# Performance work log

Hardware: AMD Instinct MI355X
Metric: run time of the kernel (lower is better)

The kernel has to match this reference:

```python
import jax, jax.numpy as jnp
import numpy as np

B, T, C = 8, 1024, 1024
H, HKV = 16, 4
HD = C // H            # 64
G = H // HKV           # 4 (GQA group size)
CAP = 50.0
THETA = 10000.0
EPS = 1e-6


def _rope_tables(t, d, theta):
    inv_freq = 1.0 / (theta ** (jnp.arange(0, d, 2, dtype=jnp.float32) / d))
    pos = jnp.arange(t, dtype=jnp.float32)
    freqs = jnp.outer(pos, inv_freq)            # [T, d/2]
    return jnp.cos(freqs), jnp.sin(freqs)


def _rmsnorm(x, w):
    var = jnp.mean(x * x, axis=-1, keepdims=True)
    return x * jax.lax.rsqrt(var + EPS) * w


def _apply_rope(x, cos, sin):
    # x: [B, T, h, HD]; cos/sin: [T, HD/2]
    d = x.shape[-1] // 2
    x1, x2 = x[..., :d], x[..., d:]
    c = cos[None, :, None, :]
    s = sin[None, :, None, :]
    return jnp.concatenate([x1 * c + x2 * s, -x1 * s + x2 * c], axis=-1)


def setup_inputs() -> dict:
    key = jax.random.key(0)
    ks = jax.random.split(key, 6)
    std = 0.02
    x = jax.random.normal(ks[0], (B, T, C), dtype=jnp.float32)
    w_q = jax.random.normal(ks[1], (C, C), dtype=jnp.float32) * std
    w_kv = jax.random.normal(ks[2], (2 * C // G, C), dtype=jnp.float32) * std  # [512, 1024]
    w_c = jax.random.normal(ks[3], (C, C), dtype=jnp.float32) * std
    q_norm_w = jnp.ones((HD,), dtype=jnp.float32)
    k_norm_w = jnp.ones((HD,), dtype=jnp.float32)
    return {"x": x, "w_q": w_q, "w_kv": w_kv, "w_c": w_c,
            "q_norm_w": q_norm_w, "k_norm_w": k_norm_w}


def reference(x, w_q, w_kv, w_c, q_norm_w, k_norm_w):
    # projections (no bias)
    q = (x @ w_q.T).reshape(B, T, H, HD)
    kv = (x @ w_kv.T).reshape(B, T, 2, HKV, HD)
    k, v = kv[:, :, 0], kv[:, :, 1]            # [B, T, HKV, HD]

    # RMSNorm on q/k heads
    q = _rmsnorm(q, q_norm_w)
    k = _rmsnorm(k, k_norm_w)

    # RoPE (half-split rotation, as in apply_rotary_emb)
    cos, sin = _rope_tables(T, HD, THETA)
    q = _apply_rope(q, cos, sin)
    k = _apply_rope(k, cos, sin)

    # GQA layout: heads grouped over kv heads (equiv to repeat_interleave)
    q = q.transpose(0, 2, 1, 3).reshape(B, HKV, G, T, HD)   # [B, nkv, G, T, HD]
    k = k.transpose(0, 2, 1, 3)                             # [B, nkv, T, HD]
    v = v.transpose(0, 2, 1, 3)

    scale = 1.0 / jnp.sqrt(jnp.float32(HD))
    att = jnp.einsum('bngqd,bnkd->bngqk', q, k) * scale     # [B, nkv, G, T, T]
    att = CAP * jnp.tanh(att / CAP)                          # soft logit cap

    causal = jnp.arange(T)[:, None] >= jnp.arange(T)[None, :]  # [T, T]
    att = jnp.where(causal[None, None, None], att, -jnp.inf)
    att = jax.nn.softmax(att, axis=-1)

    y = jnp.einsum('bngqk,bnkd->bngqd', att, v)             # [B, nkv, G, T, HD]
    y = y.reshape(B, H, T, HD).transpose(0, 2, 1, 3).reshape(B, T, C)
    return y @ w_c.T
```

## Files before the change

### kernel.cpp

```cpp
#include <hip/hip_runtime.h>
#include <math.h>

#define BB 8
#define TT 1024
#define CC 1024
#define HH 16
#define HKV 4
#define HD 64
#define MM (BB*TT)
#define LOG2E 1.4426950408889634f

typedef __attribute__((ext_vector_type(8))) short bf16x8;
typedef __attribute__((ext_vector_type(4))) float f32x4;

__device__ __forceinline__ float b2f(unsigned short x){
    union{unsigned int i; float f;} u; u.i = ((unsigned int)x)<<16; return u.f;
}
__device__ __forceinline__ unsigned short f2b(float f){
    union{float f; unsigned int i;} u; u.f = f;
    unsigned int r = u.i + 0x7fffu + ((u.i>>16)&1u);
    return (unsigned short)(r>>16);
}

#define GLD16(gp, lp) __builtin_amdgcn_global_load_lds( \
    (__attribute__((address_space(1))) void*)(gp), \
    (__attribute__((address_space(3))) void*)(lp), 16, 0, 0)

__global__ __launch_bounds__(256) void cvt_all(const float* __restrict__ x,
                                               const float* __restrict__ w_q,
                                               const float* __restrict__ w_kv,
                                               const float* __restrict__ w_c,
                                               unsigned short* __restrict__ xb,
                                               unsigned short* __restrict__ wqkvb,
                                               unsigned short* __restrict__ wcb){
    int i = blockIdx.x*256 + threadIdx.x;
    const float* src; unsigned short* dst; int off;
    if (i < 2097152)      { src = x;    dst = xb;              off = i; }
    else if (i < 2359296) { src = w_q;  dst = wqkvb;           off = i - 2097152; }
    else if (i < 2490368) { src = w_kv; dst = wqkvb + 1048576; off = i - 2359296; }
    else                  { src = w_c;  dst = wcb;             off = i - 2490368; }
    float4 f = ((const float4*)src)[off];
    ushort4 o;
    o.x = f2b(f.x); o.y = f2b(f.y); o.z = f2b(f.z); o.w = f2b(f.w);
    ((ushort4*)dst)[off] = o;
}

template<int BF16OUT>
__global__ __launch_bounds__(256, 4) void gemm_bt(const unsigned short* __restrict__ A,
                                                  const unsigned short* __restrict__ Bt,
                                                  void* __restrict__ Cc,
                                                  int M, int N, int K){
    __shared__ __align__(16) unsigned short As[128*64];
    __shared__ __align__(16) unsigned short Bs[128*64];
    const int tid  = threadIdx.x;
    const int wid  = tid >> 6;
    const int lane = tid & 63;
    const int wm   = wid >> 1;
    const int wn   = wid & 1;
    const int l16  = lane & 15;
    const int quad = lane >> 4;

    int bm, bn;
    {
        int gx = gridDim.x;
        int p  = blockIdx.y * gx + blockIdx.x;
        int nb = gx * gridDim.y;
        int l  = (p & 7) * (nb >> 3) + (p >> 3);
        bn = (l % gx) * 128;
        bm = (l / gx) * 128;
    }

    const unsigned short* ga[4]; const unsigned short* gb[4];
    char* la[4]; char* lb[4];
    {
        int rbase = tid >> 3, c_lds = tid & 7;
        #pragma unroll
        for (int it = 0; it < 4; ++it){
            int row = it*32 + rbase;
            int cg  = c_lds ^ (row & 7);
            ga[it] = A  + (size_t)(bm+row)*K + cg*8;
            gb[it] = Bt + (size_t)(bn+row)*K + cg*8;
            la[it] = (char*)As + (size_t)(it*256 + tid)*16;
            lb[it] = (char*)Bs + (size_t)(it*256 + tid)*16;
        }
    }

    f32x4 acc[4][4] = {};

    for (int k0 = 0; k0 < K; k0 += 64){
        __syncthreads();
        #pragma unroll
        for (int it = 0; it < 4; ++it){
            GLD16(ga[it] + k0, la[it]);
            GLD16(gb[it] + k0, lb[it]);
        }
        __syncthreads();

        #pragma unroll
        for (int kh = 0; kh < 2; ++kh){
            bf16x8 af[4], bfr[4];
            #pragma unroll
            for (int i = 0; i < 4; ++i){
                int row = wm*64 + i*16 + l16;
                int ch  = (kh*4 + quad) ^ (row & 7);
                af[i] = *(const bf16x8*)(As + row*64 + ch*8);
            }
            #pragma unroll
            for (int j = 0; j < 4; ++j){
                int row = wn*64 + j*16 + l16;
                int ch  = (kh*4 + quad) ^ (row & 7);
                bfr[j] = *(const bf16x8*)(Bs + row*64 + ch*8);
            }
            #pragma unroll
            for (int i = 0; i < 4; ++i)
                #pragma unroll
                for (int j = 0; j < 4; ++j)
                    acc[i][j] = __builtin_amdgcn_mfma_f32_16x16x32_bf16(af[i], bfr[j], acc[i][j], 0, 0, 0);
        }
    }

    #pragma unroll
    for (int i = 0; i < 4; ++i){
        int row0 = wm*64 + i*16 + quad*4;
        #pragma unroll
        for (int j = 0; j < 4; ++j){
            int col = bn + wn*64 + j*16 + l16;
            #pragma unroll
            for (int r = 0; r < 4; ++r){
                if (BF16OUT)
                    ((unsigned short*)Cc)[(size_t)(bm + row0 + r)*N + col] = f2b(acc[i][j][r]);
                else
                    ((float*)Cc)[(size_t)(bm + row0 + r)*N + col] = acc[i][j][r];
            }
        }
    }
}

__global__ __launch_bounds__(256) void prep_kv(const unsigned short* __restrict__ QKVb,
                                               const float* __restrict__ kw,
                                               unsigned short* __restrict__ ka,
                                               unsigned short* __restrict__ vat){
    __shared__ unsigned short tile[64][72];
    const int tid = threadIdx.x;
    const int tblk = blockIdx.x, n = blockIdx.y, b = blockIdx.z;

    #pragma unroll
    for (int it = 0; it < 2; ++it){
        int i = it*256 + tid;
        int r = i >> 3, c = i & 7;
        uint4 v = *(const uint4*)(QKVb + ((size_t)(b*TT + tblk*64 + r))*1536 + 1280 + n*64 + c*8);
        *(uint4*)(&tile[r][c*8]) = v;
    }

    {
        const int rr = tid >> 6, lane = tid & 63;
        const float kwl = kw[lane];
        const float invf = exp2f(-(float)(lane & 31) * (13.287712379549449f/32.0f));
        #pragma unroll 4
        for (int p = 0; p < 16; ++p){
            int t = tblk*64 + p*4 + rr;
            float val = b2f(QKVb[((size_t)(b*TT + t))*1536 + 1024 + n*64 + lane]);
            float ss = val*val;
            #pragma unroll
            for (int off = 32; off > 0; off >>= 1) ss += __shfl_xor(ss, off, 64);
            float normed = val * rsqrtf(ss*(1.0f/64.0f) + 1e-6f) * kwl;
            float s, c;
            sincosf((float)t * invf, &s, &c);
            float other = __shfl_xor(normed, 32, 64);
            float outv = (lane < 32) ? (normed*c + other*s) : (-other*s + normed*c);
            ka[(((size_t)(b*HKV + n))*TT + t)*HD + lane] = f2b(outv);
        }
    }

    __syncthreads();
    const int d = tid >> 2, tseg = tid & 3;
    unsigned short tmp[16];
    #pragma unroll
    for (int i = 0; i < 16; ++i) tmp[i] = tile[tseg*16 + i][d];
    size_t off = (((size_t)(b*HKV + n))*HD + d)*TT + tblk*64 + tseg*16;
    *(uint4*)(vat + off)     = *(const uint4*)tmp;
    *(uint4*)(vat + off + 8) = *(const uint4*)(tmp + 8);
}

__global__ __launch_bounds__(512, 4) void attn_mfma(const unsigned short* __restrict__ QKVb,
                                                    const unsigned short* __restrict__ ka,
                                                    const unsigned short* __restrict__ vat,
                                                    const float* __restrict__ qw,
                                                    unsigned short* __restrict__ ya){
    __shared__ __align__(16) unsigned short Ks[64*64];
    __shared__ __align__(16) unsigned short Vts[64*64];
    __shared__ __align__(16) unsigned short Ps[8][32*72];

    const int tid = threadIdx.x;
    const int wave = tid >> 6, lane = tid & 63;
    const int l16 = lane & 15, quad = lane >> 4;
    const int n = blockIdx.x, b = blockIdx.y, iz = blockIdx.z;
    const int ib = (iz < 8) ? iz : 23 - iz;
    const int head = wave & 3, sub = wave >> 2;
    const int h = n*4 + head;
    const int R0[2] = { ib*32 + sub*16, (31-ib)*32 + sub*16 };

    bf16x8 qf[2][2];
    {
        float invf[8], rw0[8], rw1[8];
        #pragma unroll
        for (int j = 0; j < 8; ++j){
            int i = quad*8 + j;
            invf[j] = exp2f(-(float)i * (13.287712379549449f/32.0f));
            rw0[j] = qw[i]; rw1[j] = qw[i + 32];
        }
        #pragma unroll
        for (int h2 = 0; h2 < 2; ++h2){
            const int t = R0[h2] + l16;
            const unsigned short* qp = QKVb + ((size_t)(b*TT + t))*1536 + h*64 + quad*8;
            float x0[8], x1[8];
            {
                uint4 a = *(const uint4*)qp;
                uint4 c = *(const uint4*)(qp + 32);
                const unsigned short* pa = (const unsigned short*)&a;
                const unsigned short* pc = (const unsigned short*)&c;
                #pragma unroll
                for (int j = 0; j < 8; ++j){ x0[j] = b2f(pa[j]); x1[j] = b2f(pc[j]); }
            }
            float ss = 0.f;
            #pragma unroll
            for (int j = 0; j < 8; ++j) ss += x0[j]*x0[j] + x1[j]*x1[j];
            ss += __shfl_xor(ss, 16, 64);
            ss += __shfl_xor(ss, 32, 64);
            float rn = rsqrtf(ss*(1.0f/64.0f) + 1e-6f);
            unsigned short o0[8], o1[8];
            #pragma unroll
            for (int j = 0; j < 8; ++j){
                float s, c;
                sincosf((float)t * invf[j], &s, &c);
                float n0 = x0[j]*rn*rw0[j];
                float n1 = x1[j]*rn*rw1[j];
                o0[j] = f2b(n0*c + n1*s);
                o1[j] = f2b(n1*c - n0*s);
            }
            qf[h2][0] = *(const bf16x8*)o0;
            qf[h2][1] = *(const bf16x8*)o1;
        }
    }

    const unsigned short* kbase = ka  + ((size_t)(b*HKV + n))*TT*HD;
    const unsigned short* vbase = vat + ((size_t)(b*HKV + n))*HD*TT;

    const unsigned short* gk; const unsigned short* gv;
    char* lk; char* lv;
    {
        int row = tid >> 3, slot = tid & 7;
        int cg = slot ^ (row & 7);
        gk = kbase + (size_t)row*HD + cg*8;
        gv = vbase + (size_t)row*TT + cg*8;
        lk = (char*)Ks  + (size_t)tid*16;
        lv = (char*)Vts + (size_t)tid*16;
    }

    f32x4 o[2][4] = {};
    f32x4 lacc[2] = {};
    unsigned short* PsW = &Ps[wave][0];

    bf16x8 ones;
    #pragma unroll
    for (int j = 0; j < 8; ++j) ones[j] = (short)0x3f80;

    const float A1 = 0.125f * LOG2E;
    const float B3 = LOG2E / 3840000.0f;
    const int sw = l16 & 7;
    const int ktmax = (1023 - 32*ib) >> 6;

    for (int kt = 0; kt <= ktmax; ++kt){
        const int k0 = kt*64;
        __syncthreads();
        GLD16(gk + (size_t)k0*HD, lk);
        GLD16(gv + k0, lv);
        __syncthreads();

        const bool act0 = (k0 <= R0[0] + 15);
        f32x4 sacc[2][4];
        __builtin_amdgcn_s_setprio(1);
        #pragma unroll
        for (int j = 0; j < 4; ++j){
            const unsigned short* kr = Ks + (j*16 + l16)*64;
            bf16x8 kf0 = *(const bf16x8*)(kr + (quad ^ sw)*8);
            bf16x8 kf1 = *(const bf16x8*)(kr + ((quad+4) ^ sw)*8);
            if (act0){
                f32x4 z = {};
                z = __builtin_amdgcn_mfma_f32_16x16x32_bf16(kf0, qf[0][0], z, 0,0,0);
                sacc[0][j] = __builtin_amdgcn_mfma_f32_16x16x32_bf16(kf1, qf[0][1], z, 0,0,0);
            }
            {
                f32x4 z = {};
                z = __builtin_amdgcn_mfma_f32_16x16x32_bf16(kf0, qf[1][0], z, 0,0,0);
                sacc[1][j] = __builtin_amdgcn_mfma_f32_16x16x32_bf16(kf1, qf[1][1], z, 0,0,0);
            }
        }
        __builtin_amdgcn_s_setprio(0);
        #pragma unroll
        for (int h2 = 0; h2 < 2; ++h2){
            if (h2 == 0 && !act0) continue;
            const int Rb = R0[h2];
            const bool full = (k0 + 63 <= Rb);
            const int qrow = Rb + l16;
            #pragma unroll
            for (int j = 0; j < 4; ++j){
                float pv[4];
                #pragma unroll
                for (int r = 0; r < 4; ++r){
                    float sr = sacc[h2][j][r];
                    float u  = sr*sr;
                    float p  = exp2f(sr * fmaf(u, -B3, A1));
                    if (!full && (k0 + j*16 + quad*4 + r > qrow)) p = 0.f;
                    pv[r] = p;
                }
                unsigned int pk0, pk1;
                asm("v_cvt_pk_bf16_f32 %0, %1, %2" : "=v"(pk0) : "v"(pv[0]), "v"(pv[1]));
                asm("v_cvt_pk_bf16_f32 %0, %1, %2" : "=v"(pk1) : "v"(pv[2]), "v"(pv[3]));
                *(uint2*)(PsW + (h2*16 + l16)*72 + j*16 + quad*4) = make_uint2(pk0, pk1);
            }
        }
        bf16x8 pf[2][2];
        if (act0){
            pf[0][0] = *(const bf16x8*)(PsW + l16*72 + quad*8);
            pf[0][1] = *(const bf16x8*)(PsW + l16*72 + quad*8 + 32);
        }
        pf[1][0] = *(const bf16x8*)(PsW + (16 + l16)*72 + quad*8);
        pf[1][1] = *(const bf16x8*)(PsW + (16 + l16)*72 + quad*8 + 32);
        __builtin_amdgcn_s_setprio(1);
        if (act0){
            lacc[0] = __builtin_amdgcn_mfma_f32_16x16x32_bf16(pf[0][0], ones, lacc[0], 0,0,0);
            lacc[0] = __builtin_amdgcn_mfma_f32_16x16x32_bf16(pf[0][1], ones, lacc[0], 0,0,0);
        }
        lacc[1] = __builtin_amdgcn_mfma_f32_16x16x32_bf16(pf[1][0], ones, lacc[1], 0,0,0);
        lacc[1] = __builtin_amdgcn_mfma_f32_16x16x32_bf16(pf[1][1], ones, lacc[1], 0,0,0);
        #pragma unroll
        for (int jd = 0; jd < 4; ++jd){
            const unsigned short* vr = Vts + (jd*16 + l16)*64;
            bf16x8 vf0 = *(const bf16x8*)(vr + (quad ^ sw)*8);
            bf16x8 vf1 = *(const bf16x8*)(vr + ((quad+4) ^ sw)*8);
            if (act0){
                o[0][jd] = __builtin_amdgcn_mfma_f32_16x16x32_bf16(pf[0][0], vf0, o[0][jd], 0,0,0);
                o[0][jd] = __builtin_amdgcn_mfma_f32_16x16x32_bf16(pf[0][1], vf1, o[0][jd], 0,0,0);
            }
            o[1][jd] = __builtin_amdgcn_mfma_f32_16x16x32_bf16(pf[1][0], vf0, o[1][jd], 0,0,0);
            o[1][jd] = __builtin_amdgcn_mfma_f32_16x16x32_bf16(pf[1][1], vf1, o[1][jd], 0,0,0);
        }
        __builtin_amdgcn_s_setprio(0);
    }

    #pragma unroll
    for (int h2 = 0; h2 < 2; ++h2){
        const int Rb = R0[h2];
        #pragma unroll
        for (int r = 0; r < 4; ++r){
            float linv = __builtin_amdgcn_rcpf(lacc[h2][r]);
            int t = Rb + quad*4 + r;
            #pragma unroll
            for (int jd = 0; jd < 4; ++jd)
                ya[(((size_t)(b*TT + t))*HH + h)*HD + jd*16 + l16] = f2b(o[h2][jd][r]*linv);
        }
    }
}

extern "C" void kernel_launch(void* const* d_in, const int* in_sizes, int n_in,
                              void* d_out, int out_size, void* d_ws, size_t ws_size,
                              hipStream_t stream) {
    const float* x    = (const float*)d_in[0];
    const float* w_q  = (const float*)d_in[1];
    const float* w_kv = (const float*)d_in[2];
    const float* w_c  = (const float*)d_in[3];
    const float* qw   = (const float*)d_in[4];
    const float* kw   = (const float*)d_in[5];
    float* out = (float*)d_out;

    char* ws = (char*)d_ws;
    unsigned short* xb    = (unsigned short*)(ws);
    unsigned short* wqkvb = (unsigned short*)(ws + ((size_t)16<<20));
    unsigned short* wcb   = (unsigned short*)(ws + ((size_t)19<<20));
    unsigned short* QKVb  = (unsigned short*)(ws + ((size_t)21<<20));
    unsigned short* ka    = (unsigned short*)(ws + ((size_t)45<<20));
    unsigned short* vat   = (unsigned short*)(ws + ((size_t)49<<20));
    unsigned short* ya    = (unsigned short*)(ws + ((size_t)53<<20));

    cvt_all<<<dim3(2752512/256), 256, 0, stream>>>(x, w_q, w_kv, w_c, xb, wqkvb, wcb);

    gemm_bt<1><<<dim3(1536/128, MM/128), 256, 0, stream>>>(xb, wqkvb, (void*)QKVb, MM, 1536, CC);

    prep_kv<<<dim3(TT/64, HKV, BB), 256, 0, stream>>>(QKVb, kw, ka, vat);

    attn_mfma<<<dim3(HKV, BB, 16), 512, 0, stream>>>(QKVb, ka, vat, qw, ya);

    gemm_bt<0><<<dim3(CC/128, MM/128), 256, 0, stream>>>(ya, wcb, (void*)out, MM, CC, CC);
}
```

Measured before the change: 206.2 us.

## Double-buffer GEMM LDS tiles with K=32 stages and vmcnt-based prefetch

Splits each 64-wide K tile of the projection GEMM into two 32-wide LDS buffers and prefetches the next half-tile with global_load_lds while the current one is consumed. Waits use s_waitcnt vmcnt with raw barriers instead of __syncthreads around every load. The LDS swizzle is changed to suit 32-element rows. The intent is to overlap global-to-LDS latency with MFMA work, at the cost of more barriers and fragile hand-counted waits.

Result: slower. 211.8 us (+2.8%).

```diff
diff --git a/kernel.cpp b/kernel.cpp
--- a/kernel.cpp
+++ b/kernel.cpp
@@ -50,8 +50,8 @@
                                                   const unsigned short* __restrict__ Bt,
                                                   void* __restrict__ Cc,
                                                   int M, int N, int K){
-    __shared__ __align__(16) unsigned short As[128*64];
-    __shared__ __align__(16) unsigned short Bs[128*64];
+    __shared__ __align__(16) unsigned short As[2][128*32];
+    __shared__ __align__(16) unsigned short Bs[2][128*32];
     const int tid  = threadIdx.x;
     const int wid  = tid >> 6;
     const int lane = tid & 63;
@@ -70,54 +70,68 @@
         bm = (l / gx) * 128;
     }
 
-    const unsigned short* ga[4]; const unsigned short* gb[4];
-    char* la[4]; char* lb[4];
+    const unsigned short* gaA; const unsigned short* gbB;
+    char* laA; char* lbB;
     {
-        int rbase = tid >> 3, c_lds = tid & 7;
-        #pragma unroll
-        for (int it = 0; it < 4; ++it){
-            int row = it*32 + rbase;
-            int cg  = c_lds ^ (row & 7);
-            ga[it] = A  + (size_t)(bm+row)*K + cg*8;
-            gb[it] = Bt + (size_t)(bn+row)*K + cg*8;
-            la[it] = (char*)As + (size_t)(it*256 + tid)*16;
-            lb[it] = (char*)Bs + (size_t)(it*256 + tid)*16;
-        }
-    }
+        int row = tid >> 2, slot = tid & 3;
+        int cg  = slot ^ ((row >> 1) & 3);
+        gaA = A  + (size_t)(bm+row)*K + cg*8;
+        gbB = Bt + (size_t)(bn+row)*K + cg*8;
+        laA = (char*)&As[0][0] + (size_t)tid*16;
+        lbB = (char*)&Bs[0][0] + (size_t)tid*16;
+    }
+    const size_t gstep = (size_t)64 * K;
 
     f32x4 acc[4][4] = {};
 
+#define STAGE32(KOFF, BOFF) do { \
+    GLD16(gaA + (KOFF),         laA + (BOFF)); \
+    GLD16(gaA + gstep + (KOFF), laA + (BOFF) + 4096); \
+    GLD16(gbB + (KOFF),         lbB + (BOFF)); \
+    GLD16(gbB + gstep + (KOFF), lbB + (BOFF) + 4096); \
+} while(0)
+
+#define COMPUTE32(ASB, BSB) do { \
+    const unsigned short* As_ = (ASB); \
+    const unsigned short* Bs_ = (BSB); \
+    bf16x8 af[4], bfr[4]; \
+    _Pragma("unroll") \
+    for (int i = 0; i < 4; ++i){ \
+        int row = wm*64 + i*16 + l16; \
+        int pc  = quad ^ ((row >> 1) & 3); \
+        af[i] = *(const bf16x8*)(As_ + row*32 + pc*8); \
+    } \
+    _Pragma("unroll") \
+    for (int j = 0; j < 4; ++j){ \
+        int row = wn*64 + j*16 + l16; \
+        int pc  = quad ^ ((row >> 1) & 3); \
+        bfr[j] = *(const bf16x8*)(Bs_ + row*32 + pc*8); \
+    } \
+    _Pragma("unroll") \
+    for (int i = 0; i < 4; ++i) \
+        _Pragma("unroll") \
+        for (int j = 0; j < 4; ++j) \
+            acc[i][j] = __builtin_amdgcn_mfma_f32_16x16x32_bf16(af[i], bfr[j], acc[i][j], 0, 0, 0); \
+} while(0)
+
+    STAGE32(0, 0);
+    STAGE32(32, 8192);
+
     for (int k0 = 0; k0 < K; k0 += 64){
-        __syncthreads();
-        #pragma unroll
-        for (int it = 0; it < 4; ++it){
-            GLD16(ga[it] + k0, la[it]);
-            GLD16(gb[it] + k0, lb[it]);
-        }
-        __syncthreads();
-
-        #pragma unroll
-        for (int kh = 0; kh < 2; ++kh){
-            bf16x8 af[4], bfr[4];
-            #pragma unroll
-            for (int i = 0; i < 4; ++i){
-                int row = wm*64 + i*16 + l16;
-                int ch  = (kh*4 + quad) ^ (row & 7);
-                af[i] = *(const bf16x8*)(As + row*64 + ch*8);
-            }
-            #pragma unroll
-            for (int j = 0; j < 4; ++j){
-                int row = wn*64 + j*16 + l16;
-                int ch  = (kh*4 + quad) ^ (row & 7);
-                bfr[j] = *(const bf16x8*)(Bs + row*64 + ch*8);
-            }
-            #pragma unroll
-            for (int i = 0; i < 4; ++i)
-                #pragma unroll
-                for (int j = 0; j < 4; ++j)
-                    acc[i][j] = __builtin_amdgcn_mfma_f32_16x16x32_bf16(af[i], bfr[j], acc[i][j], 0, 0, 0);
-        }
-    }
+        asm volatile("s_waitcnt vmcnt(4)" ::: "memory");
+        __builtin_amdgcn_s_barrier();
+        COMPUTE32(&As[0][0], &Bs[0][0]);
+        __builtin_amdgcn_s_barrier();
+        if (k0 + 64 < K) STAGE32(k0 + 64, 0);
+        if (k0 + 64 < K) asm volatile("s_waitcnt vmcnt(4)" ::: "memory");
+        else             asm volatile("s_waitcnt vmcnt(0)" ::: "memory");
+        __builtin_amdgcn_s_barrier();
+        COMPUTE32(&As[1][0], &Bs[1][0]);
+        __builtin_amdgcn_s_barrier();
+        if (k0 + 96 < K) STAGE32(k0 + 96, 8192);
+    }
+#undef STAGE32
+#undef COMPUTE32
 
     #pragma unroll
     for (int i = 0; i < 4; ++i){
```
